# Kernel optimization log

Hardware: AMD Instinct MI355X
Metric: run time of the kernel (lower is better)

The kernel has to match this reference:

```python
import jax, jax.numpy as jnp
import numpy as np

B, D, U1, U2 = 16384, 512, 512, 512
BN_EPS = 1e-3  # keras BatchNormalization default epsilon


def sparsemax(z):
    # z: [..., D]; standard sparsemax along last axis (Martins & Astudillo)
    d = z.shape[-1]
    z_sorted = -jnp.sort(-z, axis=-1)                      # descending
    z_cum = jnp.cumsum(z_sorted, axis=-1)
    k = jnp.arange(1, d + 1, dtype=z.dtype)
    support = (1.0 + k * z_sorted) > z_cum                 # [..., D] bool
    k_z = jnp.sum(support, axis=-1, keepdims=True)         # support size
    tau = (jnp.take_along_axis(z_cum, k_z.astype(jnp.int32) - 1, axis=-1) - 1.0) / k_z.astype(z.dtype)
    return jnp.maximum(z - tau, 0.0)


def setup_inputs() -> dict:
    key = jax.random.key(0)
    ks = jax.random.split(key, 8)
    x = jax.random.normal(ks[0], (B, D), dtype=jnp.float32)
    W1 = jax.random.normal(ks[1], (D, U1), dtype=jnp.float32) * 0.05
    b1 = jnp.zeros((U1,), jnp.float32)
    centers = jax.random.normal(ks[2], (U2, D), dtype=jnp.float32)      # paraboloid centers
    coefs = jax.random.normal(ks[3], (U2, D), dtype=jnp.float32) * 0.1  # paraboloid axis coefficients
    bn_gamma = jnp.ones((D,), jnp.float32)
    bn_beta = jnp.zeros((D,), jnp.float32)
    bn_mean = jnp.zeros((D,), jnp.float32)
    bn_var = jnp.ones((D,), jnp.float32)
    W_out = jax.random.normal(ks[4], (U1 + U2, D), dtype=jnp.float32) * 0.05
    b_out = jnp.zeros((D,), jnp.float32)
    w_add = jnp.array([0.5, 0.5], jnp.float32)  # WeightedAdd learnable scalars
    return {"x": x, "W1": W1, "b1": b1, "centers": centers, "coefs": coefs,
            "bn_gamma": bn_gamma, "bn_beta": bn_beta, "bn_mean": bn_mean, "bn_var": bn_var,
            "W_out": W_out, "b_out": b_out, "w_add": w_add}


def reference(x, W1, b1, centers, coefs, bn_gamma, bn_beta, bn_mean, bn_var, W_out, b_out, w_add):
    # Dense branch
    h1 = jax.nn.relu(x @ W1 + b1)                               # [B, U1]
    # BoundedParaboloids branch: BatchNorm (inference stats) then bounded paraboloids
    xb = (x - bn_mean) * jax.lax.rsqrt(bn_var + BN_EPS) * bn_gamma + bn_beta
    # q_j = sum_d (coefs[j,d] * (xb_d - centers[j,d]))^2, computed via GEMMs
    A = coefs * coefs                                            # [U2, D]
    q = (xb * xb) @ A.T - 2.0 * (xb @ (A * centers).T) + jnp.sum(A * centers * centers, axis=-1)
    h2 = jax.nn.relu(1.0 - q)                                    # [B, U2] bounded paraboloids
    # Output embedding: Dense(relu) on concat
    emb = jax.nn.relu(jnp.concatenate([h1, h2], axis=-1) @ W_out + b_out)  # [B, D]
    # WeightedAdd of (dropout-identity) inputs and embedding; dropout_rate=0 / inference
    pre = w_add[0] * x + w_add[1] * emb
    mask = sparsemax(pre)                                        # [B, D]
    return mask
```

## Files before the change

kernel.cpp:

```cpp
#include <hip/hip_runtime.h>
#include <math.h>

typedef float f4 __attribute__((ext_vector_type(4)));
typedef float f32x4 __attribute__((ext_vector_type(4)));
typedef __bf16 bf16x8 __attribute__((ext_vector_type(8)));
typedef unsigned short u16;
typedef u16 us8 __attribute__((ext_vector_type(8)));

__device__ __forceinline__ u16 f2bf(float f) {
  unsigned u = __builtin_bit_cast(unsigned, f);
  unsigned r = u + 0x7fffu + ((u >> 16) & 1u);
  return (u16)(r >> 16);
}
__device__ __forceinline__ float bf2f(u16 h) {
  unsigned u = ((unsigned)h) << 16;
  return __builtin_bit_cast(float, u);
}

__global__ __launch_bounds__(256) void prep_bn_kernel(
    const float* __restrict__ gamma, const float* __restrict__ beta,
    const float* __restrict__ mean, const float* __restrict__ var,
    float* __restrict__ scale, float* __restrict__ shift) {
  int d = blockIdx.x * blockDim.x + threadIdx.x;
  if (d < 512) {
    float s = rsqrtf(var[d] + 1e-3f) * gamma[d];
    scale[d] = s;
    shift[d] = beta[d] - mean[d] * s;
  }
}

__global__ __launch_bounds__(64) void prep_params_kernel(
    const float* __restrict__ coefs, const float* __restrict__ centers,
    u16* __restrict__ pth, float* __restrict__ cvec) {
  int j = blockIdx.x;
  int l = threadIdx.x;
  int d0 = l * 8;
  f4 c0 = *(const f4*)(coefs + (size_t)j * 512 + d0);
  f4 c1 = *(const f4*)(coefs + (size_t)j * 512 + d0 + 4);
  f4 e0 = *(const f4*)(centers + (size_t)j * 512 + d0);
  f4 e1 = *(const f4*)(centers + (size_t)j * 512 + d0 + 4);
  us8 pa, pb;
  float acc = 0.f;
#pragma unroll
  for (int e = 0; e < 8; ++e) {
    float cf = (e < 4) ? c0[e] : c1[e - 4];
    float ce = (e < 4) ? e0[e] : e1[e - 4];
    float a = cf * cf;
    pa[e] = f2bf(a);
    pb[e] = f2bf(-2.f * a * ce);
    acc = fmaf(a * ce, ce, acc);
  }
  *(us8*)(pth + (size_t)j * 1024 + d0) = pa;
  *(us8*)(pth + (size_t)j * 1024 + 512 + d0) = pb;
#pragma unroll
  for (int off = 32; off; off >>= 1) acc += __shfl_xor(acc, off);
  if (l == 0) cvec[j] = acc;
}

__global__ __launch_bounds__(256) void transpose_split_kernel(
    const float* __restrict__ in, u16* __restrict__ th, int K, int N) {
  __shared__ float t[32][33];
  int lx = threadIdx.x;
  int ly = threadIdx.y;
  int n0 = blockIdx.x * 32, k0 = blockIdx.y * 32;
#pragma unroll
  for (int i = 0; i < 4; ++i)
    t[ly + 8 * i][lx] = in[(size_t)(k0 + ly + 8 * i) * N + n0 + lx];
  __syncthreads();
#pragma unroll
  for (int i = 0; i < 4; ++i) {
    float v = t[lx][ly + 8 * i];
    th[(size_t)(n0 + ly + 8 * i) * K + k0 + lx] = f2bf(v);
  }
}

__global__ __launch_bounds__(256) void conv_x_kernel(
    const float* __restrict__ x, const float* __restrict__ scale,
    const float* __restrict__ shift, u16* __restrict__ xh,
    u16* __restrict__ xb, u16* __restrict__ xsq) {
  int gid = blockIdx.x * 256 + threadIdx.x;
  int m = gid >> 6;
  int d0 = (gid & 63) * 8;
  f4 v0 = *(const f4*)(x + (size_t)m * 512 + d0);
  f4 v1 = *(const f4*)(x + (size_t)m * 512 + d0 + 4);
  f4 s0 = *(const f4*)(scale + d0);
  f4 s1 = *(const f4*)(scale + d0 + 4);
  f4 h0 = *(const f4*)(shift + d0);
  f4 h1 = *(const f4*)(shift + d0 + 4);
  us8 oh, ob, oq;
#pragma unroll
  for (int e = 0; e < 8; ++e) {
    float xv = (e < 4) ? v0[e] : v1[e - 4];
    float sc = (e < 4) ? s0[e] : s1[e - 4];
    float sh = (e < 4) ? h0[e] : h1[e - 4];
    oh[e] = f2bf(xv);
    float xbf = fmaf(xv, sc, sh);
    ob[e] = f2bf(xbf);
    oq[e] = f2bf(xbf * xbf);
  }
  *(us8*)(xh + (size_t)m * 512 + d0) = oh;
  *(us8*)(xb + (size_t)m * 512 + d0) = ob;
  *(us8*)(xsq + (size_t)m * 512 + d0) = oq;
}

__device__ __forceinline__ void wait_vm8() {
  asm volatile("s_waitcnt vmcnt(8)" ::: "memory");
}
__device__ __forceinline__ void wait_vm0() {
  asm volatile("s_waitcnt vmcnt(0)" ::: "memory");
}
__device__ __forceinline__ void sbar() { __builtin_amdgcn_s_barrier(); }
__device__ __forceinline__ void sgb0() { __builtin_amdgcn_sched_barrier(0); }

__global__ __launch_bounds__(256, 2) void gemm_fused12(
    const u16* __restrict__ Xh, const u16* __restrict__ Xb,
    const u16* __restrict__ Xsq, const u16* __restrict__ W1th,
    const u16* __restrict__ Pth, const float* __restrict__ b1,
    const float* __restrict__ cvec, u16* __restrict__ Hout) {
  extern __shared__ char smem[];
  const int tid = threadIdx.x;
  const int l = tid & 63;
  const int w = tid >> 6;
  const int wm = w & 1, wn = w >> 1;
  const int lr = l & 15, lk = l >> 4;
  const int sx = lr & 7;
  const int bid = blockIdx.x;
  const int L = (bid & 7) * 128 + (bid >> 3);
  const int p = L >> 3;
  const int g = ((L >> 2) & 1) ^ 1;
  const int n = L & 3;
  const int m0 = p * 128, n0 = n * 128;
  const int Kg = g ? 1024 : 512;
  const int nt = g ? 16 : 8;
  const u16* Bmat = g ? Pth : W1th;
  const int srow = l >> 3;
  const int sslot = (l & 7) ^ srow;

  f32x4 acc[4][4];
#pragma unroll
  for (int i = 0; i < 4; ++i)
#pragma unroll
    for (int j = 0; j < 4; ++j) acc[i][j] = (f32x4){0.f, 0.f, 0.f, 0.f};

#define F12_STAGE(buf, k0)                                                    \
  {                                                                           \
    const u16* Asrc = g ? (((k0) < 512) ? Xsq : Xb) : Xh;                     \
    const int kb = (k0)&511;                                                  \
    char* dA = smem + (buf)*16384;                                            \
    char* dB = smem + 32768 + (buf)*16384;                                    \
    _Pragma("unroll") for (int pp = 0; pp < 4; ++pp) {                        \
      int c = pp * 4 + w;                                                     \
      int row = c * 8 + srow;                                                 \
      int loff = c * 1024;                                                    \
      size_t goa = (size_t)(m0 + row) * 512 + kb + sslot * 8;                 \
      size_t gob = (size_t)(n0 + row) * Kg + (k0) + sslot * 8;                \
      __builtin_amdgcn_global_load_lds(                                       \
          (const __attribute__((address_space(1))) void*)(Asrc + goa),        \
          (__attribute__((address_space(3))) void*)(dA + loff), 16, 0, 0);    \
      __builtin_amdgcn_global_load_lds(                                       \
          (const __attribute__((address_space(1))) void*)(Bmat + gob),        \
          (__attribute__((address_space(3))) void*)(dB + loff), 16, 0, 0);    \
    }                                                                         \
  }

  F12_STAGE(0, 0);
  F12_STAGE(1, 64);
  for (int t = 0; t < nt; ++t) {
    if (t + 1 < nt) {
      wait_vm8();
    } else {
      wait_vm0();
    }
    sgb0();
    sbar();
    sgb0();
    const char* sA = smem + (t & 1) * 16384;
    const char* sB = smem + 32768 + (t & 1) * 16384;
#pragma unroll
    for (int ks = 0; ks < 2; ++ks) {
      bf16x8 av[4], bv[4];
#pragma unroll
      for (int i = 0; i < 4; ++i)
        av[i] = *(const bf16x8*)(sA + (wm * 64 + i * 16 + lr) * 128 +
                                 (((ks * 4 + lk) ^ sx) * 16));
#pragma unroll
      for (int j = 0; j < 4; ++j)
        bv[j] = *(const bf16x8*)(sB + (wn * 64 + j * 16 + lr) * 128 +
                                 (((ks * 4 + lk) ^ sx) * 16));
#pragma unroll
      for (int i = 0; i < 4; ++i)
#pragma unroll
        for (int j = 0; j < 4; ++j)
          acc[i][j] = __builtin_amdgcn_mfma_f32_16x16x32_bf16(av[i], bv[j],
                                                              acc[i][j], 0, 0, 0);
    }
    sgb0();
    sbar();
    sgb0();
    if (t + 2 < nt) F12_STAGE(t & 1, (t + 2) * 64);
  }
#undef F12_STAGE

  const int mwb = m0 + wm * 64;
  const int nwb = n0 + wn * 64;
  const float* bias = g ? cvec : b1;
#pragma unroll
  for (int j = 0; j < 4; ++j) {
    int nn = nwb + j * 16 + lr;
    float bv = bias[nn];
#pragma unroll
    for (int i = 0; i < 4; ++i) {
#pragma unroll
      for (int r = 0; r < 4; ++r) {
        int m = mwb + i * 16 + lk * 4 + r;
        float v = acc[i][j][r] + bv;
        v = g ? fmaxf(1.f - v, 0.f) : fmaxf(v, 0.f);
        Hout[(size_t)m * 1024 + g * 512 + nn] = f2bf(v);
      }
    }
  }
}

__global__ __launch_bounds__(256, 2) void gemm3(
    const u16* __restrict__ Ah, const u16* __restrict__ Bh,
    const float* __restrict__ bias, const float* __restrict__ xorig,
    const float* __restrict__ wadd, float* __restrict__ outp) {
  extern __shared__ char smem[];
  const int tid = threadIdx.x;
  const int l = tid & 63;
  const int w = tid >> 6;
  const int wm = w & 1, wn = w >> 1;
  const int lr = l & 15, lk = l >> 4;
  const int sx = lr & 7;
  const int bid = blockIdx.x;
  const int lin = (bid & 7) * 64 + (bid >> 3);
  const int m0 = (lin >> 2) * 128, n0 = (lin & 3) * 128;
  const int srow = l >> 3;
  const int sslot = (l & 7) ^ srow;

  f32x4 acc[4][4];
#pragma unroll
  for (int i = 0; i < 4; ++i)
#pragma unroll
    for (int j = 0; j < 4; ++j) acc[i][j] = (f32x4){0.f, 0.f, 0.f, 0.f};

#define G3_STAGE(buf, k0)                                                     \
  {                                                                           \
    char* dA = smem + (buf)*16384;                                            \
    char* dB = smem + 32768 + (buf)*16384;                                    \
    _Pragma("unroll") for (int pp = 0; pp < 4; ++pp) {                        \
      int c = pp * 4 + w;                                                     \
      int row = c * 8 + srow;                                                 \
      int loff = c * 1024;                                                    \
      size_t gob = (size_t)(n0 + row) * 1024 + (k0) + sslot * 8;              \
      size_t goa = (size_t)(m0 + row) * 1024 + (k0) + sslot * 8;              \
      __builtin_amdgcn_global_load_lds(                                       \
          (const __attribute__((address_space(1))) void*)(Bh + gob),          \
          (__attribute__((address_space(3))) void*)(dB + loff), 16, 0, 0);    \
      __builtin_amdgcn_global_load_lds(                                       \
          (const __attribute__((address_space(1))) void*)(Ah + goa),          \
          (__attribute__((address_space(3))) void*)(dA + loff), 16, 0, 0);    \
    }                                                                         \
  }

  G3_STAGE(0, 0);
  G3_STAGE(1, 64);
  for (int t = 0; t < 16; ++t) {
    if (t + 1 < 16) {
      wait_vm8();
    } else {
      wait_vm0();
    }
    sgb0();
    sbar();
    sgb0();
    const char* sA = smem + (t & 1) * 16384;
    const char* sB = smem + 32768 + (t & 1) * 16384;
#pragma unroll
    for (int ks = 0; ks < 2; ++ks) {
      bf16x8 av[4], bv[4];
#pragma unroll
      for (int i = 0; i < 4; ++i)
        av[i] = *(const bf16x8*)(sA + (wm * 64 + i * 16 + lr) * 128 +
                                 (((ks * 4 + lk) ^ sx) * 16));
#pragma unroll
      for (int j = 0; j < 4; ++j)
        bv[j] = *(const bf16x8*)(sB + (wn * 64 + j * 16 + lr) * 128 +
                                 (((ks * 4 + lk) ^ sx) * 16));
#pragma unroll
      for (int i = 0; i < 4; ++i)
#pragma unroll
        for (int j = 0; j < 4; ++j)
          acc[i][j] = __builtin_amdgcn_mfma_f32_16x16x32_bf16(av[i], bv[j],
                                                              acc[i][j], 0, 0, 0);
    }
    sgb0();
    sbar();
    sgb0();
    if (t + 2 < 16) G3_STAGE(t & 1, (t + 2) * 64);
  }
#undef G3_STAGE

  const int mwb = m0 + wm * 64;
  const int nwb = n0 + wn * 64;
  float w0 = wadd[0], w1 = wadd[1];
#pragma unroll
  for (int j = 0; j < 4; ++j) {
    int n = nwb + j * 16 + lr;
    float bv = bias[n];
#pragma unroll
    for (int i = 0; i < 4; ++i) {
#pragma unroll
      for (int r = 0; r < 4; ++r) {
        int m = mwb + i * 16 + lk * 4 + r;
        float v = fmaxf(acc[i][j][r] + bv, 0.f);
        outp[(size_t)m * 512 + n] = fmaf(w1, v, w0 * xorig[(size_t)m * 512 + n]);
      }
    }
  }
}

__global__ __launch_bounds__(256) void sparsemax_kernel(float* __restrict__ out) {
  int wrk = (blockIdx.x & 7) * 512 + (blockIdx.x >> 3);
  int row = wrk * 4 + (threadIdx.x >> 6);
  int lane = threadIdx.x & 63;
  float* rp = out + (size_t)row * 512;
  f4 z0 = *(const f4*)(rp + lane * 8);
  f4 z1 = *(const f4*)(rp + lane * 8 + 4);
  float z[8];
#pragma unroll
  for (int e = 0; e < 4; ++e) {
    z[e] = z0[e];
    z[4 + e] = z1[e];
  }
  float m = z[0];
#pragma unroll
  for (int i = 1; i < 8; ++i) m = fmaxf(m, z[i]);
#pragma unroll
  for (int off = 32; off; off >>= 1) m = fmaxf(m, __shfl_xor(m, off));
  float tau = m - 1.0f;
  for (int it = 0; it < 32; ++it) {
    float s = 0.f, k = 0.f;
#pragma unroll
    for (int i = 0; i < 8; ++i) {
      if (z[i] > tau) {
        s += z[i] - tau;
        k += 1.f;
      }
    }
#pragma unroll
    for (int off = 32; off; off >>= 1) {
      s += __shfl_xor(s, off);
      k += __shfl_xor(k, off);
    }
    if (k < 0.5f) break;
    float tn = tau + (s - 1.f) / k;
    if (tn == tau) break;
    tau = tn;
  }
  float s = 0.f, k = 0.f;
#pragma unroll
  for (int i = 0; i < 8; ++i)
    if (z[i] > tau) {
      s += z[i];
      k += 1.f;
    }
#pragma unroll
  for (int off = 32; off; off >>= 1) {
    s += __shfl_xor(s, off);
    k += __shfl_xor(k, off);
  }
  float tauf = (k >= 0.5f) ? (s - 1.f) / k : (m - 1.f);
  f4 o0, o1;
#pragma unroll
  for (int e = 0; e < 4; ++e) {
    o0[e] = fmaxf(z[e] - tauf, 0.f);
    o1[e] = fmaxf(z[4 + e] - tauf, 0.f);
  }
  *(f4*)(rp + lane * 8) = o0;
  *(f4*)(rp + lane * 8 + 4) = o1;
}

extern "C" void kernel_launch(void* const* d_in, const int* in_sizes, int n_in,
                              void* d_out, int out_size, void* d_ws,
                              size_t ws_size, hipStream_t stream) {
  const float* x = (const float*)d_in[0];
  const float* W1 = (const float*)d_in[1];
  const float* b1 = (const float*)d_in[2];
  const float* centers = (const float*)d_in[3];
  const float* coefs = (const float*)d_in[4];
  const float* gamma = (const float*)d_in[5];
  const float* beta = (const float*)d_in[6];
  const float* mean = (const float*)d_in[7];
  const float* var = (const float*)d_in[8];
  const float* W_out = (const float*)d_in[9];
  const float* b_out = (const float*)d_in[10];
  const float* wadd = (const float*)d_in[11];
  float* out = (float*)d_out;

  char* ws = (char*)d_ws;
  u16* Hh = (u16*)(ws);
  u16* Xh = (u16*)(ws + 33554432);
  u16* Xb = (u16*)(ws + 50331648);
  char* pool = ws + 67108864;
  u16* W1th = (u16*)(pool);
  u16* Pth = (u16*)(pool + 1048576);
  float* cvec = (float*)(ws + 69206016);
  float* scale = (float*)(ws + 69208064);
  float* shift = (float*)(ws + 69210112);
  u16* Xsq = (u16*)d_out;
  const bool bigws = (ws_size >= (size_t)70260736);
  u16* Wth = bigws ? (u16*)(ws + 69212160) : (u16*)(pool);

  prep_bn_kernel<<<2, 256, 0, stream>>>(gamma, beta, mean, var, scale, shift);
  prep_params_kernel<<<512, 64, 0, stream>>>(coefs, centers, Pth, cvec);
  transpose_split_kernel<<<dim3(16, 16), dim3(32, 8), 0, stream>>>(W1, W1th,
                                                                   512, 512);
  if (bigws) {
    transpose_split_kernel<<<dim3(16, 32), dim3(32, 8), 0, stream>>>(
        W_out, Wth, 1024, 512);
  }
  conv_x_kernel<<<4096, 256, 0, stream>>>(x, scale, shift, Xh, Xb, Xsq);

  gemm_fused12<<<1024, 256, 65536, stream>>>(Xh, Xb, Xsq, W1th, Pth, b1, cvec,
                                             Hh);

  if (!bigws) {
    transpose_split_kernel<<<dim3(16, 32), dim3(32, 8), 0, stream>>>(
        W_out, Wth, 1024, 512);
  }
  gemm3<<<512, 256, 65536, stream>>>(Hh, Wth, b_out, x, wadd, out);
  sparsemax_kernel<<<4096, 256, 0, stream>>>(out);
}
```

Baseline: 106.3 us.

## Merge prep kernels into one launch and fold BN into W1 weights

Replaces the five small prep launches with a single block-range-dispatched kernel. The dense-branch GEMM now reads the batch-normalized bf16 activations instead of a separate bf16 copy of x. W1 is divided by the BN scale during transpose and the bias is adjusted so the result is unchanged. This drops one 16 MB bf16 activation write and several launch gaps. It risks precision loss, and division by a BN scale near zero if gamma is small, and the bias-adjust blocks compute rsqrt serially in a loop.

```diff
diff --git a/kernel.cpp b/kernel.cpp
--- a/kernel.cpp
+++ b/kernel.cpp
@@ -7,6 +7,8 @@
 typedef unsigned short u16;
 typedef u16 us8 __attribute__((ext_vector_type(8)));
 
+#define BN_EPS 1e-3f
+
 __device__ __forceinline__ u16 f2bf(float f) {
   unsigned u = __builtin_bit_cast(unsigned, f);
   unsigned r = u + 0x7fffu + ((u >> 16) & 1u);
@@ -17,90 +19,121 @@
   return __builtin_bit_cast(float, u);
 }
 
-__global__ __launch_bounds__(256) void prep_bn_kernel(
-    const float* __restrict__ gamma, const float* __restrict__ beta,
-    const float* __restrict__ mean, const float* __restrict__ var,
-    float* __restrict__ scale, float* __restrict__ shift) {
-  int d = blockIdx.x * blockDim.x + threadIdx.x;
-  if (d < 512) {
-    float s = rsqrtf(var[d] + 1e-3f) * gamma[d];
-    scale[d] = s;
-    shift[d] = beta[d] - mean[d] * s;
-  }
-}
-
-__global__ __launch_bounds__(64) void prep_params_kernel(
-    const float* __restrict__ coefs, const float* __restrict__ centers,
-    u16* __restrict__ pth, float* __restrict__ cvec) {
-  int j = blockIdx.x;
-  int l = threadIdx.x;
-  int d0 = l * 8;
-  f4 c0 = *(const f4*)(coefs + (size_t)j * 512 + d0);
-  f4 c1 = *(const f4*)(coefs + (size_t)j * 512 + d0 + 4);
-  f4 e0 = *(const f4*)(centers + (size_t)j * 512 + d0);
-  f4 e1 = *(const f4*)(centers + (size_t)j * 512 + d0 + 4);
-  us8 pa, pb;
-  float acc = 0.f;
-#pragma unroll
-  for (int e = 0; e < 8; ++e) {
-    float cf = (e < 4) ? c0[e] : c1[e - 4];
-    float ce = (e < 4) ? e0[e] : e1[e - 4];
-    float a = cf * cf;
-    pa[e] = f2bf(a);
-    pb[e] = f2bf(-2.f * a * ce);
-    acc = fmaf(a * ce, ce, acc);
-  }
-  *(us8*)(pth + (size_t)j * 1024 + d0) = pa;
-  *(us8*)(pth + (size_t)j * 1024 + 512 + d0) = pb;
-#pragma unroll
-  for (int off = 32; off; off >>= 1) acc += __shfl_xor(acc, off);
-  if (l == 0) cvec[j] = acc;
-}
-
-__global__ __launch_bounds__(256) void transpose_split_kernel(
-    const float* __restrict__ in, u16* __restrict__ th, int K, int N) {
-  __shared__ float t[32][33];
-  int lx = threadIdx.x;
-  int ly = threadIdx.y;
-  int n0 = blockIdx.x * 32, k0 = blockIdx.y * 32;
-#pragma unroll
-  for (int i = 0; i < 4; ++i)
-    t[ly + 8 * i][lx] = in[(size_t)(k0 + ly + 8 * i) * N + n0 + lx];
-  __syncthreads();
-#pragma unroll
-  for (int i = 0; i < 4; ++i) {
-    float v = t[lx][ly + 8 * i];
-    th[(size_t)(n0 + ly + 8 * i) * K + k0 + lx] = f2bf(v);
-  }
-}
-
-__global__ __launch_bounds__(256) void conv_x_kernel(
-    const float* __restrict__ x, const float* __restrict__ scale,
-    const float* __restrict__ shift, u16* __restrict__ xh,
-    u16* __restrict__ xb, u16* __restrict__ xsq) {
-  int gid = blockIdx.x * 256 + threadIdx.x;
-  int m = gid >> 6;
-  int d0 = (gid & 63) * 8;
-  f4 v0 = *(const f4*)(x + (size_t)m * 512 + d0);
-  f4 v1 = *(const f4*)(x + (size_t)m * 512 + d0 + 4);
-  f4 s0 = *(const f4*)(scale + d0);
-  f4 s1 = *(const f4*)(scale + d0 + 4);
-  f4 h0 = *(const f4*)(shift + d0);
-  f4 h1 = *(const f4*)(shift + d0 + 4);
-  us8 oh, ob, oq;
-#pragma unroll
-  for (int e = 0; e < 8; ++e) {
-    float xv = (e < 4) ? v0[e] : v1[e - 4];
-    float sc = (e < 4) ? s0[e] : s1[e - 4];
-    float sh = (e < 4) ? h0[e] : h1[e - 4];
-    oh[e] = f2bf(xv);
-    float xbf = fmaf(xv, sc, sh);
-    ob[e] = f2bf(xbf);
-    oq[e] = f2bf(xbf * xbf);
-  }
-  *(us8*)(xh + (size_t)m * 512 + d0) = oh;
-  *(us8*)(xb + (size_t)m * 512 + d0) = ob;
-  *(us8*)(xsq + (size_t)m * 512 + d0) = oq;
+__global__ __launch_bounds__(256) void prep_all_kernel(
+    const float* __restrict__ x, const float* __restrict__ W1,
+    const float* __restrict__ b1, const float* __restrict__ centers,
+    const float* __restrict__ coefs, const float* __restrict__ gamma,
+    const float* __restrict__ beta, const float* __restrict__ mean,
+    const float* __restrict__ var, const float* __restrict__ W_out,
+    u16* __restrict__ Xb, u16* __restrict__ Xsq, u16* __restrict__ Pth,
+    float* __restrict__ cvec, u16* __restrict__ W1th, u16* __restrict__ Wth,
+    float* __restrict__ b1a) {
+  __shared__ float tsh[32][33];
+  __shared__ float red[4][64];
+  const int bid = blockIdx.x;
+  const int tid = threadIdx.x;
+
+  if (bid < 4096) {
+    int gid = bid * 256 + tid;
+    int m = gid >> 6;
+    int d0 = (gid & 63) * 8;
+    f4 v0 = *(const f4*)(x + (size_t)m * 512 + d0);
+    f4 v1 = *(const f4*)(x + (size_t)m * 512 + d0 + 4);
+    f4 g0 = *(const f4*)(gamma + d0);
+    f4 g1 = *(const f4*)(gamma + d0 + 4);
+    f4 be0 = *(const f4*)(beta + d0);
+    f4 be1 = *(const f4*)(beta + d0 + 4);
+    f4 mn0 = *(const f4*)(mean + d0);
+    f4 mn1 = *(const f4*)(mean + d0 + 4);
+    f4 va0 = *(const f4*)(var + d0);
+    f4 va1 = *(const f4*)(var + d0 + 4);
+    us8 ob, oq;
+#pragma unroll
+    for (int e = 0; e < 8; ++e) {
+      float xv = (e < 4) ? v0[e] : v1[e - 4];
+      float gv = (e < 4) ? g0[e] : g1[e - 4];
+      float bv = (e < 4) ? be0[e] : be1[e - 4];
+      float mv = (e < 4) ? mn0[e] : mn1[e - 4];
+      float vv = (e < 4) ? va0[e] : va1[e - 4];
+      float s = rsqrtf(vv + BN_EPS) * gv;
+      float sh = bv - mv * s;
+      float xbf = fmaf(xv, s, sh);
+      ob[e] = f2bf(xbf);
+      oq[e] = f2bf(xbf * xbf);
+    }
+    *(us8*)(Xb + (size_t)m * 512 + d0) = ob;
+    *(us8*)(Xsq + (size_t)m * 512 + d0) = oq;
+  } else if (bid < 4608) {
+    int j = bid - 4096;
+    int d = tid * 2;
+    float acc = 0.f;
+    u16 pa2[2], pb2[2];
+#pragma unroll
+    for (int e = 0; e < 2; ++e) {
+      float cf = coefs[(size_t)j * 512 + d + e];
+      float ce = centers[(size_t)j * 512 + d + e];
+      float a = cf * cf;
+      pa2[e] = f2bf(a);
+      pb2[e] = f2bf(-2.f * a * ce);
+      acc = fmaf(a * ce, ce, acc);
+    }
+    *(unsigned*)(Pth + (size_t)j * 1024 + d) =
+        ((unsigned)pa2[1] << 16) | pa2[0];
+    *(unsigned*)(Pth + (size_t)j * 1024 + 512 + d) =
+        ((unsigned)pb2[1] << 16) | pb2[0];
+#pragma unroll
+    for (int off = 32; off; off >>= 1) acc += __shfl_xor(acc, off);
+    if ((tid & 63) == 0) red[0][tid >> 6] = acc;
+    __syncthreads();
+    if (tid == 0)
+      cvec[j] = red[0][0] + red[0][1] + red[0][2] + red[0][3];
+  } else if (bid < 4864) {
+    int i = bid - 4608;
+    int lx = tid & 31, ly = tid >> 5;
+    int n0 = (i & 15) * 32, k0 = (i >> 4) * 32;
+#pragma unroll
+    for (int q = 0; q < 4; ++q)
+      tsh[ly + 8 * q][lx] = W1[(size_t)(k0 + ly + 8 * q) * 512 + n0 + lx];
+    __syncthreads();
+    int k = k0 + lx;
+    float s = rsqrtf(var[k] + BN_EPS) * gamma[k];
+#pragma unroll
+    for (int q = 0; q < 4; ++q) {
+      float v = tsh[lx][ly + 8 * q] / s;
+      W1th[(size_t)(n0 + ly + 8 * q) * 512 + k] = f2bf(v);
+    }
+  } else if (bid < 5376) {
+    int i = bid - 4864;
+    int lx = tid & 31, ly = tid >> 5;
+    int n0 = (i & 15) * 32, k0 = (i >> 4) * 32;
+#pragma unroll
+    for (int q = 0; q < 4; ++q)
+      tsh[ly + 8 * q][lx] = W_out[(size_t)(k0 + ly + 8 * q) * 512 + n0 + lx];
+    __syncthreads();
+#pragma unroll
+    for (int q = 0; q < 4; ++q) {
+      float v = tsh[lx][ly + 8 * q];
+      Wth[(size_t)(n0 + ly + 8 * q) * 1024 + k0 + lx] = f2bf(v);
+    }
+  } else {
+    int b = bid - 5376;
+    int lane = tid & 63;
+    int kq = tid >> 6;
+    int j = b * 64 + lane;
+    float partial = 0.f;
+    for (int i = 0; i < 128; ++i) {
+      int k = kq * 128 + i;
+      float s = rsqrtf(var[k] + BN_EPS) * gamma[k];
+      float sh = beta[k] - mean[k] * s;
+      partial = fmaf(sh, W1[(size_t)k * 512 + j] / s, partial);
+    }
+    red[kq][lane] = partial;
+    __syncthreads();
+    if (tid < 64) {
+      float t = red[0][tid] + red[1][tid] + red[2][tid] + red[3][tid];
+      b1a[b * 64 + tid] = b1[b * 64 + tid] - t;
+    }
+  }
 }
 
 __device__ __forceinline__ void wait_vm8() {
@@ -113,10 +146,10 @@
 __device__ __forceinline__ void sgb0() { __builtin_amdgcn_sched_barrier(0); }
 
 __global__ __launch_bounds__(256, 2) void gemm_fused12(
-    const u16* __restrict__ Xh, const u16* __restrict__ Xb,
-    const u16* __restrict__ Xsq, const u16* __restrict__ W1th,
-    const u16* __restrict__ Pth, const float* __restrict__ b1,
-    const float* __restrict__ cvec, u16* __restrict__ Hout) {
+    const u16* __restrict__ Xb, const u16* __restrict__ Xsq,
+    const u16* __restrict__ W1th, const u16* __restrict__ Pth,
+    const float* __restrict__ b1a, const float* __restrict__ cvec,
+    u16* __restrict__ Hout) {
   extern __shared__ char smem[];
   const int tid = threadIdx.x;
   const int l = tid & 63;
@@ -144,7 +177,7 @@
 
 #define F12_STAGE(buf, k0)                                                    \
   {                                                                           \
-    const u16* Asrc = g ? (((k0) < 512) ? Xsq : Xb) : Xh;                     \
+    const u16* Asrc = g ? (((k0) < 512) ? Xsq : Xb) : Xb;                     \
     const int kb = (k0)&511;                                                  \
     char* dA = smem + (buf)*16384;                                            \
     char* dB = smem + 32768 + (buf)*16384;                                    \
@@ -203,7 +236,7 @@
 
   const int mwb = m0 + wm * 64;
   const int nwb = n0 + wn * 64;
-  const float* bias = g ? cvec : b1;
+  const float* bias = g ? cvec : b1a;
 #pragma unroll
   for (int j = 0; j < 4; ++j) {
     int nn = nwb + j * 16 + lr;
@@ -400,35 +433,21 @@
 
   char* ws = (char*)d_ws;
   u16* Hh = (u16*)(ws);
-  u16* Xh = (u16*)(ws + 33554432);
+  float* b1a = (float*)(ws + 33554432);
+  u16* Wth = (u16*)(ws + 33562624);
   u16* Xb = (u16*)(ws + 50331648);
   char* pool = ws + 67108864;
   u16* W1th = (u16*)(pool);
   u16* Pth = (u16*)(pool + 1048576);
   float* cvec = (float*)(ws + 69206016);
-  float* scale = (float*)(ws + 69208064);
-  float* shift = (float*)(ws + 69210112);
   u16* Xsq = (u16*)d_out;
-  const bool bigws = (ws_size >= (size_t)70260736);
-  u16* Wth = bigws ? (u16*)(ws + 69212160) : (u16*)(pool);
-
-  prep_bn_kernel<<<2, 256, 0, stream>>>(gamma, beta, mean, var, scale, shift);
-  prep_params_kernel<<<512, 64, 0, stream>>>(coefs, centers, Pth, cvec);
-  transpose_split_kernel<<<dim3(16, 16), dim3(32, 8), 0, stream>>>(W1, W1th,
-                                                                   512, 512);
-  if (bigws) {
-    transpose_split_kernel<<<dim3(16, 32), dim3(32, 8), 0, stream>>>(
-        W_out, Wth, 1024, 512);
-  }
-  conv_x_kernel<<<4096, 256, 0, stream>>>(x, scale, shift, Xh, Xb, Xsq);
-
-  gemm_fused12<<<1024, 256, 65536, stream>>>(Xh, Xb, Xsq, W1th, Pth, b1, cvec,
+
+  prep_all_kernel<<<5384, 256, 0, stream>>>(x, W1, b1, centers, coefs, gamma,
+                                            beta, mean, var, W_out, Xb, Xsq,
+                                            Pth, cvec, W1th, Wth, b1a);
+
+  gemm_fused12<<<1024, 256, 65536, stream>>>(Xb, Xsq, W1th, Pth, b1a, cvec,
                                              Hh);
-
-  if (!bigws) {
-    transpose_split_kernel<<<dim3(16, 32), dim3(32, 8), 0, stream>>>(
-        W_out, Wth, 1024, 512);
-  }
   gemm3<<<512, 256, 65536, stream>>>(Hh, Wth, b_out, x, wadd, out);
   sparsemax_kernel<<<4096, 256, 0, stream>>>(out);
 }
```

New measurement: 108.8 us. 1.02x slower.
